# Kernel optimization log

Hardware: AMD Instinct MI355X
Metric: run time of the kernel (lower is better)

## Reference

```python
import jax, jax.numpy as jnp
import numpy as np

WEIGHT = 0.01

def setup_inputs() -> dict:
    key = jax.random.key(0)
    k1, k2 = jax.random.split(key)
    shape = jax.random.normal(k1, (16, 4096, 3), dtype=jnp.float32)
    template = jax.random.normal(k2, (16, 4096, 3), dtype=jnp.float32)
    return {"shape": shape, "template": template}

def _chamfer(pred, target):
    # Euclidean cdist via the |x|^2 + |y|^2 - 2<x,y> expansion to avoid a (B,M,N,3) tensor.
    p2 = jnp.sum(pred * pred, axis=-1)          # (B, M)
    t2 = jnp.sum(target * target, axis=-1)      # (B, N)
    cross = jnp.einsum('bmd,bnd->bmn', pred, target)  # (B, M, N)
    d2 = p2[:, :, None] + t2[None if p2.ndim == 1 else slice(None), None, :] - 2.0 * cross
    dist = jnp.sqrt(jnp.maximum(d2, 0.0))       # (B, M, N) euclidean, matches torch.cdist
    min_p2t = jnp.min(dist, axis=2)             # (B, M)
    min_t2p = jnp.min(dist, axis=1)             # (B, N)
    chamfer = jnp.sum(min_p2t, axis=1) + jnp.sum(min_t2p, axis=1)  # (B,)
    return jnp.mean(chamfer)                    # reduction='mean'

def reference(shape, template):
    return WEIGHT * _chamfer(shape, template)
```

## Files before the change

kernel.cpp:

```cpp
#include <hip/hip_runtime.h>

#define NPTS 4096
#define NBATCH 16
#define THREADS 256
#define QPB 256
#define TCH 1024
#define NCH (NPTS / TCH)

typedef __attribute__((ext_vector_type(8))) short short8;
typedef __attribute__((ext_vector_type(16))) float float16v;

static __device__ __forceinline__ unsigned short f2bf(float f) {
  unsigned int u = __builtin_bit_cast(unsigned int, f);
  u = (u + 0x7FFFu + ((u >> 16) & 1u)) >> 16;
  return (unsigned short)u;
}
static __device__ __forceinline__ float bf2f(unsigned short h) {
  unsigned int u = ((unsigned int)h) << 16;
  return __builtin_bit_cast(float, u);
}
static __device__ __forceinline__ int toff(int j, int h) {
  return (j * 16 + h * 8) ^ (((j >> 2) & 7) << 3);
}

__global__ __launch_bounds__(THREADS)
__attribute__((amdgpu_waves_per_eu(2, 2)))
void chamfer_mfma(const float* __restrict__ shape,
                  const float* __restrict__ tmpl,
                  float* __restrict__ out) {
  __shared__ unsigned short tgt[TCH * 16];
  __shared__ unsigned short qry[QPB * 16];
  __shared__ float p2s[QPB];
  __shared__ float redbuf[4];

  const int qc = blockIdx.x;
  const int b = blockIdx.y;
  const int dir = blockIdx.z;
  const float* Pb = (dir == 0 ? shape : tmpl) + (size_t)b * NPTS * 3;
  const float* Tb = (dir == 0 ? tmpl : shape) + (size_t)b * NPTS * 3;

  const int tid = threadIdx.x;
  const int lane = tid & 63;
  const int wave = tid >> 6;
  const int n = lane & 31;
  const int kg = lane >> 5;

  {
    const int qg = qc * QPB + tid;
    const float px = Pb[3 * qg + 0], py = Pb[3 * qg + 1], pz = Pb[3 * qg + 2];
    const float ux = -2.0f * px, uy = -2.0f * py, uz = -2.0f * pz;
    const unsigned short hx = f2bf(ux), hy = f2bf(uy), hz = f2bf(uz);
    const unsigned short lx = f2bf(ux - bf2f(hx)), ly = f2bf(uy - bf2f(hy)),
                         lz = f2bf(uz - bf2f(hz));
    const unsigned short ONE = 0x3F80;
    short8 v0, v1;
    v0[0] = hx; v0[1] = hx; v0[2] = lx; v0[3] = hy;
    v0[4] = hy; v0[5] = ly; v0[6] = hz; v0[7] = hz;
    v1[0] = lz; v1[1] = ONE; v1[2] = ONE; v1[3] = 0;
    v1[4] = 0;  v1[5] = 0;  v1[6] = 0;  v1[7] = 0;
    *(short8*)&qry[tid * 16] = v0;
    *(short8*)&qry[tid * 16 + 8] = v1;
    p2s[tid] = fmaf(px, px, fmaf(py, py, pz * pz));
  }
  __syncthreads();

  const short8 af0 = *(const short8*)&qry[(wave * 64 + n) * 16 + kg * 8];
  const short8 af1 = *(const short8*)&qry[(wave * 64 + 32 + n) * 16 + kg * 8];

  const float INF = 3.402823466e38f;
  float acc0[16], acc1[16];
  #pragma unroll
  for (int r = 0; r < 16; ++r) { acc0[r] = INF; acc1[r] = INF; }

  const float4* T4 = (const float4*)Tb;
  for (int ch = 0; ch < NCH; ++ch) {
    __syncthreads();
    {
      const int g = ch * (TCH / 4) + tid;
      const float4 a = T4[g * 3 + 0];
      const float4 c = T4[g * 3 + 1];
      const float4 d = T4[g * 3 + 2];
      const float X[4] = {a.x, a.w, c.z, d.y};
      const float Y[4] = {a.y, c.x, c.w, d.z};
      const float Z[4] = {a.z, c.y, d.x, d.w};
      #pragma unroll
      for (int p = 0; p < 4; ++p) {
        const float x = X[p], y = Y[p], z = Z[p];
        const float t2 = fmaf(x, x, fmaf(y, y, z * z));
        const unsigned short hx = f2bf(x), hy = f2bf(y), hz = f2bf(z);
        const unsigned short lx = f2bf(x - bf2f(hx)), ly = f2bf(y - bf2f(hy)),
                             lz = f2bf(z - bf2f(hz));
        const unsigned short h2 = f2bf(t2), l2 = f2bf(t2 - bf2f(h2));
        short8 v0, v1;
        v0[0] = hx; v0[1] = lx; v0[2] = hx; v0[3] = hy;
        v0[4] = ly; v0[5] = hy; v0[6] = hz; v0[7] = lz;
        v1[0] = hz; v1[1] = h2; v1[2] = l2; v1[3] = 0;
        v1[4] = 0;  v1[5] = 0;  v1[6] = 0;  v1[7] = 0;
        const int j = tid * 4 + p;
        *(short8*)&tgt[toff(j, 0)] = v0;
        *(short8*)&tgt[toff(j, 1)] = v1;
      }
    }
    __syncthreads();

    for (int tp = 0; tp < TCH / 64; ++tp) {
      const short8 b0 = *(const short8*)&tgt[toff(tp * 64 + n, kg)];
      const short8 b1 = *(const short8*)&tgt[toff(tp * 64 + 32 + n, kg)];
      const float16v z = {};
      float16v d00 = __builtin_amdgcn_mfma_f32_32x32x16_bf16(af0, b0, z, 0, 0, 0);
      float16v d10 = __builtin_amdgcn_mfma_f32_32x32x16_bf16(af1, b0, z, 0, 0, 0);
      float16v d01 = __builtin_amdgcn_mfma_f32_32x32x16_bf16(af0, b1, z, 0, 0, 0);
      float16v d11 = __builtin_amdgcn_mfma_f32_32x32x16_bf16(af1, b1, z, 0, 0, 0);
      #pragma unroll
      for (int r = 0; r < 16; ++r)
        acc0[r] = fminf(fminf(d00[r], d01[r]), acc0[r]);
      #pragma unroll
      for (int r = 0; r < 16; ++r)
        acc1[r] = fminf(fminf(d10[r], d11[r]), acc1[r]);
    }
  }

  #pragma unroll
  for (int m = 1; m <= 16; m <<= 1) {
    #pragma unroll
    for (int r = 0; r < 16; ++r) {
      acc0[r] = fminf(acc0[r], __shfl_xor(acc0[r], m, 64));
      acc1[r] = fminf(acc1[r], __shfl_xor(acc1[r], m, 64));
    }
  }

  float s = 0.0f;
  if (n == 0) {
    const int qb = wave * 64;
    #pragma unroll
    for (int r = 0; r < 16; ++r) {
      const int row = (r & 3) + 8 * (r >> 2) + 4 * kg;
      s += sqrtf(fmaxf(acc0[r] + p2s[qb + row], 0.0f));
      s += sqrtf(fmaxf(acc1[r] + p2s[qb + 32 + row], 0.0f));
    }
  }
  s += __shfl_xor(s, 32, 64);
  if (lane == 0) redbuf[wave] = s;
  __syncthreads();
  if (tid == 0) {
    atomicAdd(out, (redbuf[0] + redbuf[1] + redbuf[2] + redbuf[3]) * (0.01f / 16.0f));
  }
}

extern "C" void kernel_launch(void* const* d_in, const int* in_sizes, int n_in,
                              void* d_out, int out_size, void* d_ws, size_t ws_size,
                              hipStream_t stream) {
  const float* shape = (const float*)d_in[0];
  const float* tmpl = (const float*)d_in[1];
  float* out = (float*)d_out;

  hipMemsetAsync(out, 0, sizeof(float) * out_size, stream);

  dim3 grid(NPTS / QPB, NBATCH, 2);
  chamfer_mfma<<<grid, dim3(THREADS), 0, stream>>>(shape, tmpl, out);
}
```

Before: 81.88 us.

## Split target set across blocks with workspace combine kernel and fold query norm into MFMA

Splits each query tile's target scan into two halves handled by separate blocks, which doubles the grid. Per-query partial minima go to a workspace, and a second kernel takes the min, applies sqrt, and reduces with a ticket-based last-block sum. This replaces the memset and atomic accumulation. The query norm is folded into the MFMA operands so no p2 add is needed afterwards, and the occupancy hint is raised to 4 waves per EU. A scalar fallback kernel handles the case where the workspace is too small. The change aims to fill the machine better but adds a second launch and workspace traffic.

```diff
diff --git a/kernel.cpp b/kernel.cpp
--- a/kernel.cpp
+++ b/kernel.cpp
@@ -4,8 +4,11 @@
 #define NBATCH 16
 #define THREADS 256
 #define QPB 256
-#define TCH 1024
-#define NCH (NPTS / TCH)
+#define TH 2
+#define TGH (NPTS / TH)
+#define TCH 512
+#define NCH (TGH / TCH)
+#define NBLK_B 512
 
 typedef __attribute__((ext_vector_type(8))) short short8;
 typedef __attribute__((ext_vector_type(16))) float float16v;
@@ -22,18 +25,22 @@
 static __device__ __forceinline__ int toff(int j, int h) {
   return (j * 16 + h * 8) ^ (((j >> 2) & 7) << 3);
 }
+#define WSIDX(b, dir, th, q) (((((b)*2 + (dir)) * 2 + (th)) << 12) + (q))
 
 __global__ __launch_bounds__(THREADS)
-__attribute__((amdgpu_waves_per_eu(2, 2)))
+__attribute__((amdgpu_waves_per_eu(4, 4)))
 void chamfer_mfma(const float* __restrict__ shape,
                   const float* __restrict__ tmpl,
-                  float* __restrict__ out) {
+                  float* __restrict__ ws,
+                  unsigned int* __restrict__ ticket) {
   __shared__ unsigned short tgt[TCH * 16];
   __shared__ unsigned short qry[QPB * 16];
-  __shared__ float p2s[QPB];
-  __shared__ float redbuf[4];
-
-  const int qc = blockIdx.x;
+
+  if (blockIdx.x == 0 && blockIdx.y == 0 && blockIdx.z == 0 && threadIdx.x == 0)
+    *ticket = 0u;
+
+  const int qc = blockIdx.x >> 1;
+  const int th = blockIdx.x & 1;
   const int b = blockIdx.y;
   const int dir = blockIdx.z;
   const float* Pb = (dir == 0 ? shape : tmpl) + (size_t)b * NPTS * 3;
@@ -49,18 +56,19 @@
     const int qg = qc * QPB + tid;
     const float px = Pb[3 * qg + 0], py = Pb[3 * qg + 1], pz = Pb[3 * qg + 2];
     const float ux = -2.0f * px, uy = -2.0f * py, uz = -2.0f * pz;
+    const float p2 = fmaf(px, px, fmaf(py, py, pz * pz));
     const unsigned short hx = f2bf(ux), hy = f2bf(uy), hz = f2bf(uz);
     const unsigned short lx = f2bf(ux - bf2f(hx)), ly = f2bf(uy - bf2f(hy)),
                          lz = f2bf(uz - bf2f(hz));
+    const unsigned short h2 = f2bf(p2), l2 = f2bf(p2 - bf2f(h2));
     const unsigned short ONE = 0x3F80;
     short8 v0, v1;
     v0[0] = hx; v0[1] = hx; v0[2] = lx; v0[3] = hy;
     v0[4] = hy; v0[5] = ly; v0[6] = hz; v0[7] = hz;
-    v1[0] = lz; v1[1] = ONE; v1[2] = ONE; v1[3] = 0;
-    v1[4] = 0;  v1[5] = 0;  v1[6] = 0;  v1[7] = 0;
+    v1[0] = lz; v1[1] = ONE; v1[2] = ONE; v1[3] = h2;
+    v1[4] = l2; v1[5] = 0;  v1[6] = 0;  v1[7] = 0;
     *(short8*)&qry[tid * 16] = v0;
     *(short8*)&qry[tid * 16 + 8] = v1;
-    p2s[tid] = fmaf(px, px, fmaf(py, py, pz * pz));
   }
   __syncthreads();
 
@@ -71,12 +79,13 @@
   float acc0[16], acc1[16];
   #pragma unroll
   for (int r = 0; r < 16; ++r) { acc0[r] = INF; acc1[r] = INF; }
+  const float16v z = {};
 
   const float4* T4 = (const float4*)Tb;
   for (int ch = 0; ch < NCH; ++ch) {
     __syncthreads();
-    {
-      const int g = ch * (TCH / 4) + tid;
+    if (tid < TCH / 4) {
+      const int g = th * (TGH / 4) + ch * (TCH / 4) + tid;
       const float4 a = T4[g * 3 + 0];
       const float4 c = T4[g * 3 + 1];
       const float4 d = T4[g * 3 + 2];
@@ -85,17 +94,18 @@
       const float Z[4] = {a.z, c.y, d.x, d.w};
       #pragma unroll
       for (int p = 0; p < 4; ++p) {
-        const float x = X[p], y = Y[p], z = Z[p];
-        const float t2 = fmaf(x, x, fmaf(y, y, z * z));
-        const unsigned short hx = f2bf(x), hy = f2bf(y), hz = f2bf(z);
+        const float x = X[p], y = Y[p], zc = Z[p];
+        const float t2 = fmaf(x, x, fmaf(y, y, zc * zc));
+        const unsigned short hx = f2bf(x), hy = f2bf(y), hz = f2bf(zc);
         const unsigned short lx = f2bf(x - bf2f(hx)), ly = f2bf(y - bf2f(hy)),
-                             lz = f2bf(z - bf2f(hz));
+                             lz = f2bf(zc - bf2f(hz));
         const unsigned short h2 = f2bf(t2), l2 = f2bf(t2 - bf2f(h2));
+        const unsigned short ONE = 0x3F80;
         short8 v0, v1;
         v0[0] = hx; v0[1] = lx; v0[2] = hx; v0[3] = hy;
         v0[4] = ly; v0[5] = hy; v0[6] = hz; v0[7] = lz;
-        v1[0] = hz; v1[1] = h2; v1[2] = l2; v1[3] = 0;
-        v1[4] = 0;  v1[5] = 0;  v1[6] = 0;  v1[7] = 0;
+        v1[0] = hz; v1[1] = h2; v1[2] = l2; v1[3] = ONE;
+        v1[4] = ONE; v1[5] = 0; v1[6] = 0; v1[7] = 0;
         const int j = tid * 4 + p;
         *(short8*)&tgt[toff(j, 0)] = v0;
         *(short8*)&tgt[toff(j, 1)] = v1;
@@ -103,20 +113,24 @@
     }
     __syncthreads();
 
+    #pragma unroll 2
     for (int tp = 0; tp < TCH / 64; ++tp) {
       const short8 b0 = *(const short8*)&tgt[toff(tp * 64 + n, kg)];
       const short8 b1 = *(const short8*)&tgt[toff(tp * 64 + 32 + n, kg)];
-      const float16v z = {};
-      float16v d00 = __builtin_amdgcn_mfma_f32_32x32x16_bf16(af0, b0, z, 0, 0, 0);
-      float16v d10 = __builtin_amdgcn_mfma_f32_32x32x16_bf16(af1, b0, z, 0, 0, 0);
-      float16v d01 = __builtin_amdgcn_mfma_f32_32x32x16_bf16(af0, b1, z, 0, 0, 0);
-      float16v d11 = __builtin_amdgcn_mfma_f32_32x32x16_bf16(af1, b1, z, 0, 0, 0);
-      #pragma unroll
-      for (int r = 0; r < 16; ++r)
-        acc0[r] = fminf(fminf(d00[r], d01[r]), acc0[r]);
-      #pragma unroll
-      for (int r = 0; r < 16; ++r)
-        acc1[r] = fminf(fminf(d10[r], d11[r]), acc1[r]);
+      {
+        float16v d0 = __builtin_amdgcn_mfma_f32_32x32x16_bf16(af0, b0, z, 0, 0, 0);
+        float16v d1 = __builtin_amdgcn_mfma_f32_32x32x16_bf16(af0, b1, z, 0, 0, 0);
+        #pragma unroll
+        for (int r = 0; r < 16; ++r)
+          acc0[r] = fminf(fminf(d0[r], d1[r]), acc0[r]);
+      }
+      {
+        float16v d0 = __builtin_amdgcn_mfma_f32_32x32x16_bf16(af1, b0, z, 0, 0, 0);
+        float16v d1 = __builtin_amdgcn_mfma_f32_32x32x16_bf16(af1, b1, z, 0, 0, 0);
+        #pragma unroll
+        for (int r = 0; r < 16; ++r)
+          acc1[r] = fminf(fminf(d0[r], d1[r]), acc1[r]);
+      }
     }
   }
 
@@ -129,22 +143,102 @@
     }
   }
 
-  float s = 0.0f;
   if (n == 0) {
-    const int qb = wave * 64;
+    const int qbase = qc * QPB + wave * 64;
+    const int wsb = WSIDX(b, dir, th, 0);
     #pragma unroll
     for (int r = 0; r < 16; ++r) {
       const int row = (r & 3) + 8 * (r >> 2) + 4 * kg;
-      s += sqrtf(fmaxf(acc0[r] + p2s[qb + row], 0.0f));
-      s += sqrtf(fmaxf(acc1[r] + p2s[qb + 32 + row], 0.0f));
-    }
-  }
-  s += __shfl_xor(s, 32, 64);
-  if (lane == 0) redbuf[wave] = s;
-  __syncthreads();
-  if (tid == 0) {
-    atomicAdd(out, (redbuf[0] + redbuf[1] + redbuf[2] + redbuf[3]) * (0.01f / 16.0f));
-  }
+      ws[wsb + qbase + row] = acc0[r];
+      ws[wsb + qbase + 32 + row] = acc1[r];
+    }
+  }
+}
+
+__global__ __launch_bounds__(THREADS) void chamfer_combine(
+    const float* __restrict__ ws, float* __restrict__ partials,
+    unsigned int* __restrict__ ticket, float* __restrict__ out) {
+  __shared__ float red[4];
+  __shared__ bool amLast;
+  const int g = blockIdx.x * THREADS + threadIdx.x;
+  const int b = g >> 13;
+  const int dir = (g >> 12) & 1;
+  const int q = g & 4095;
+
+  const float m = fminf(ws[WSIDX(b, dir, 0, q)], ws[WSIDX(b, dir, 1, q)]);
+  float s = sqrtf(fmaxf(m, 0.0f));
+
+  #pragma unroll
+  for (int off = 32; off > 0; off >>= 1) s += __shfl_down(s, off, 64);
+  const int lane = threadIdx.x & 63;
+  const int wid = threadIdx.x >> 6;
+  if (lane == 0) red[wid] = s;
+  __syncthreads();
+  if (threadIdx.x == 0) {
+    partials[blockIdx.x] = red[0] + red[1] + red[2] + red[3];
+    __threadfence();
+    unsigned int t = atomicAdd(ticket, 1u);
+    amLast = (t == (unsigned int)(gridDim.x - 1));
+  }
+  __syncthreads();
+  if (amLast) {
+    __threadfence();
+    float v = partials[threadIdx.x] + partials[threadIdx.x + THREADS];
+    #pragma unroll
+    for (int off = 32; off > 0; off >>= 1) v += __shfl_down(v, off, 64);
+    if (lane == 0) red[wid] = v;
+    __syncthreads();
+    if (threadIdx.x == 0)
+      out[0] = (red[0] + red[1] + red[2] + red[3]) * (0.01f / 16.0f);
+  }
+}
+
+__global__ __launch_bounds__(THREADS) void chamfer_fallback(
+    const float* __restrict__ shape, const float* __restrict__ tmpl,
+    float* __restrict__ out) {
+  __shared__ float4 tile[NPTS];
+  const int b = blockIdx.y;
+  const int dir = blockIdx.z;
+  const float* Pb = (dir == 0 ? shape : tmpl) + (size_t)b * NPTS * 3;
+  const float* Tb = (dir == 0 ? tmpl : shape) + (size_t)b * NPTS * 3;
+  const float4* T4 = (const float4*)Tb;
+  for (int base = threadIdx.x * 4; base < NPTS; base += THREADS * 4) {
+    const int k = base >> 2;
+    float4 a = T4[3 * k + 0], c = T4[3 * k + 1], d = T4[3 * k + 2];
+    tile[base + 0] = make_float4(a.x, a.y, a.z, 0.5f * fmaf(a.x, a.x, fmaf(a.y, a.y, a.z * a.z)));
+    tile[base + 1] = make_float4(a.w, c.x, c.y, 0.5f * fmaf(a.w, a.w, fmaf(c.x, c.x, c.y * c.y)));
+    tile[base + 2] = make_float4(c.z, c.w, d.x, 0.5f * fmaf(c.z, c.z, fmaf(c.w, c.w, d.x * d.x)));
+    tile[base + 3] = make_float4(d.y, d.z, d.w, 0.5f * fmaf(d.y, d.y, fmaf(d.z, d.z, d.w * d.w)));
+  }
+  __syncthreads();
+  const int m0 = blockIdx.x * (THREADS * 2) + threadIdx.x;
+  const int m1 = m0 + THREADS;
+  const float qx0 = Pb[3 * m0], qy0 = Pb[3 * m0 + 1], qz0 = Pb[3 * m0 + 2];
+  const float qx1 = Pb[3 * m1], qy1 = Pb[3 * m1 + 1], qz1 = Pb[3 * m1 + 2];
+  const float nx0 = -qx0, ny0 = -qy0, nz0 = -qz0;
+  const float nx1 = -qx1, ny1 = -qy1, nz1 = -qz1;
+  const float p20 = fmaf(qx0, qx0, fmaf(qy0, qy0, qz0 * qz0));
+  const float p21 = fmaf(qx1, qx1, fmaf(qy1, qy1, qz1 * qz1));
+  const float INF = 3.402823466e38f;
+  float a00 = INF, a01 = INF, a10 = INF, a11 = INF;
+  #pragma unroll 2
+  for (int n = 0; n < NPTS; n += 2) {
+    float4 t0 = tile[n], t1 = tile[n + 1];
+    a00 = fminf(a00, fmaf(nx0, t0.x, fmaf(ny0, t0.y, fmaf(nz0, t0.z, t0.w))));
+    a10 = fminf(a10, fmaf(nx1, t0.x, fmaf(ny1, t0.y, fmaf(nz1, t0.z, t0.w))));
+    a01 = fminf(a01, fmaf(nx0, t1.x, fmaf(ny0, t1.y, fmaf(nz0, t1.z, t1.w))));
+    a11 = fminf(a11, fmaf(nx1, t1.x, fmaf(ny1, t1.y, fmaf(nz1, t1.z, t1.w))));
+  }
+  float s = sqrtf(fmaxf(fmaf(2.0f, fminf(a00, a01), p20), 0.0f)) +
+            sqrtf(fmaxf(fmaf(2.0f, fminf(a10, a11), p21), 0.0f));
+  #pragma unroll
+  for (int off = 32; off > 0; off >>= 1) s += __shfl_down(s, off, 64);
+  __syncthreads();
+  float* red = (float*)tile;
+  if ((threadIdx.x & 63) == 0) red[threadIdx.x >> 6] = s;
+  __syncthreads();
+  if (threadIdx.x == 0)
+    atomicAdd(out, (red[0] + red[1] + red[2] + red[3]) * (0.01f / 16.0f));
 }
 
 extern "C" void kernel_launch(void* const* d_in, const int* in_sizes, int n_in,
@@ -154,8 +248,19 @@
   const float* tmpl = (const float*)d_in[1];
   float* out = (float*)d_out;
 
-  hipMemsetAsync(out, 0, sizeof(float) * out_size, stream);
-
-  dim3 grid(NPTS / QPB, NBATCH, 2);
-  chamfer_mfma<<<grid, dim3(THREADS), 0, stream>>>(shape, tmpl, out);
-}
+  const size_t ws_mins = (size_t)NBATCH * 2 * TH * NPTS * sizeof(float);
+  const size_t ws_needed = ws_mins + NBLK_B * sizeof(float) + sizeof(unsigned int);
+  if (ws_size >= ws_needed) {
+    float* ws_part = (float*)d_ws;
+    float* partials = (float*)((char*)d_ws + ws_mins);
+    unsigned int* ticket = (unsigned int*)(partials + NBLK_B);
+    dim3 gridA(16 * TH, NBATCH, 2);
+    chamfer_mfma<<<gridA, dim3(THREADS), 0, stream>>>(shape, tmpl, ws_part, ticket);
+    chamfer_combine<<<dim3(NBLK_B), dim3(THREADS), 0, stream>>>(
+        ws_part, partials, ticket, out);
+  } else {
+    hipMemsetAsync(out, 0, sizeof(float) * out_size, stream);
+    dim3 grid(NPTS / (THREADS * 2), NBATCH, 2);
+    chamfer_fallback<<<grid, dim3(THREADS), 0, stream>>>(shape, tmpl, out);
+  }
+}
```

After: 91.30 us. 11.5% more time.

## Halve query tile per block and fold query norm into MFMA K dimension

Applied to the files above, without the earlier changes.

Cuts queries per block from 256 to 128, so each wave handles one 32-row MFMA tile instead of two. This doubles the grid and raises the occupancy target to 4 waves per EU. The query squared norm is now split into hi/lo bf16 terms and placed in spare K slots of the dot-product vector, paired with ONE entries on the target side, so the MFMA output already holds the full squared distance. That removes the p2s shared array and the epilogue add. In exchange, each block stages the full target set into shared memory for half as many queries, which doubles the total target conversion work and LDS traffic.

```diff
diff --git a/kernel.cpp b/kernel.cpp
--- a/kernel.cpp
+++ b/kernel.cpp
@@ -3,7 +3,7 @@
 #define NPTS 4096
 #define NBATCH 16
 #define THREADS 256
-#define QPB 256
+#define QPB 128
 #define TCH 1024
 #define NCH (NPTS / TCH)
 
@@ -24,13 +24,12 @@
 }
 
 __global__ __launch_bounds__(THREADS)
-__attribute__((amdgpu_waves_per_eu(2, 2)))
+__attribute__((amdgpu_waves_per_eu(4, 4)))
 void chamfer_mfma(const float* __restrict__ shape,
                   const float* __restrict__ tmpl,
                   float* __restrict__ out) {
   __shared__ unsigned short tgt[TCH * 16];
   __shared__ unsigned short qry[QPB * 16];
-  __shared__ float p2s[QPB];
   __shared__ float redbuf[4];
 
   const int qc = blockIdx.x;
@@ -45,32 +44,33 @@
   const int n = lane & 31;
   const int kg = lane >> 5;
 
-  {
+  if (tid < QPB) {
     const int qg = qc * QPB + tid;
     const float px = Pb[3 * qg + 0], py = Pb[3 * qg + 1], pz = Pb[3 * qg + 2];
     const float ux = -2.0f * px, uy = -2.0f * py, uz = -2.0f * pz;
+    const float p2 = fmaf(px, px, fmaf(py, py, pz * pz));
     const unsigned short hx = f2bf(ux), hy = f2bf(uy), hz = f2bf(uz);
     const unsigned short lx = f2bf(ux - bf2f(hx)), ly = f2bf(uy - bf2f(hy)),
                          lz = f2bf(uz - bf2f(hz));
+    const unsigned short h2 = f2bf(p2), l2 = f2bf(p2 - bf2f(h2));
     const unsigned short ONE = 0x3F80;
     short8 v0, v1;
     v0[0] = hx; v0[1] = hx; v0[2] = lx; v0[3] = hy;
     v0[4] = hy; v0[5] = ly; v0[6] = hz; v0[7] = hz;
-    v1[0] = lz; v1[1] = ONE; v1[2] = ONE; v1[3] = 0;
-    v1[4] = 0;  v1[5] = 0;  v1[6] = 0;  v1[7] = 0;
+    v1[0] = lz; v1[1] = ONE; v1[2] = ONE; v1[3] = h2;
+    v1[4] = l2; v1[5] = 0;  v1[6] = 0;  v1[7] = 0;
     *(short8*)&qry[tid * 16] = v0;
     *(short8*)&qry[tid * 16 + 8] = v1;
-    p2s[tid] = fmaf(px, px, fmaf(py, py, pz * pz));
   }
   __syncthreads();
 
-  const short8 af0 = *(const short8*)&qry[(wave * 64 + n) * 16 + kg * 8];
-  const short8 af1 = *(const short8*)&qry[(wave * 64 + 32 + n) * 16 + kg * 8];
+  const short8 af = *(const short8*)&qry[(wave * 32 + n) * 16 + kg * 8];
 
   const float INF = 3.402823466e38f;
-  float acc0[16], acc1[16];
+  float acc[16];
   #pragma unroll
-  for (int r = 0; r < 16; ++r) { acc0[r] = INF; acc1[r] = INF; }
+  for (int r = 0; r < 16; ++r) acc[r] = INF;
+  const float16v z = {};
 
   const float4* T4 = (const float4*)Tb;
   for (int ch = 0; ch < NCH; ++ch) {
@@ -85,17 +85,18 @@
       const float Z[4] = {a.z, c.y, d.x, d.w};
       #pragma unroll
       for (int p = 0; p < 4; ++p) {
-        const float x = X[p], y = Y[p], z = Z[p];
-        const float t2 = fmaf(x, x, fmaf(y, y, z * z));
-        const unsigned short hx = f2bf(x), hy = f2bf(y), hz = f2bf(z);
+        const float x = X[p], y = Y[p], zc = Z[p];
+        const float t2 = fmaf(x, x, fmaf(y, y, zc * zc));
+        const unsigned short hx = f2bf(x), hy = f2bf(y), hz = f2bf(zc);
         const unsigned short lx = f2bf(x - bf2f(hx)), ly = f2bf(y - bf2f(hy)),
-                             lz = f2bf(z - bf2f(hz));
+                             lz = f2bf(zc - bf2f(hz));
         const unsigned short h2 = f2bf(t2), l2 = f2bf(t2 - bf2f(h2));
+        const unsigned short ONE = 0x3F80;
         short8 v0, v1;
         v0[0] = hx; v0[1] = lx; v0[2] = hx; v0[3] = hy;
         v0[4] = ly; v0[5] = hy; v0[6] = hz; v0[7] = lz;
-        v1[0] = hz; v1[1] = h2; v1[2] = l2; v1[3] = 0;
-        v1[4] = 0;  v1[5] = 0;  v1[6] = 0;  v1[7] = 0;
+        v1[0] = hz; v1[1] = h2; v1[2] = l2; v1[3] = ONE;
+        v1[4] = ONE; v1[5] = 0; v1[6] = 0; v1[7] = 0;
         const int j = tid * 4 + p;
         *(short8*)&tgt[toff(j, 0)] = v0;
         *(short8*)&tgt[toff(j, 1)] = v1;
@@ -106,38 +107,26 @@
     for (int tp = 0; tp < TCH / 64; ++tp) {
       const short8 b0 = *(const short8*)&tgt[toff(tp * 64 + n, kg)];
       const short8 b1 = *(const short8*)&tgt[toff(tp * 64 + 32 + n, kg)];
-      const float16v z = {};
-      float16v d00 = __builtin_amdgcn_mfma_f32_32x32x16_bf16(af0, b0, z, 0, 0, 0);
-      float16v d10 = __builtin_amdgcn_mfma_f32_32x32x16_bf16(af1, b0, z, 0, 0, 0);
-      float16v d01 = __builtin_amdgcn_mfma_f32_32x32x16_bf16(af0, b1, z, 0, 0, 0);
-      float16v d11 = __builtin_amdgcn_mfma_f32_32x32x16_bf16(af1, b1, z, 0, 0, 0);
+      float16v d0 = __builtin_amdgcn_mfma_f32_32x32x16_bf16(af, b0, z, 0, 0, 0);
+      float16v d1 = __builtin_amdgcn_mfma_f32_32x32x16_bf16(af, b1, z, 0, 0, 0);
       #pragma unroll
       for (int r = 0; r < 16; ++r)
-        acc0[r] = fminf(fminf(d00[r], d01[r]), acc0[r]);
-      #pragma unroll
-      for (int r = 0; r < 16; ++r)
-        acc1[r] = fminf(fminf(d10[r], d11[r]), acc1[r]);
+        acc[r] = fminf(fminf(d0[r], d1[r]), acc[r]);
     }
   }
 
   #pragma unroll
   for (int m = 1; m <= 16; m <<= 1) {
     #pragma unroll
-    for (int r = 0; r < 16; ++r) {
-      acc0[r] = fminf(acc0[r], __shfl_xor(acc0[r], m, 64));
-      acc1[r] = fminf(acc1[r], __shfl_xor(acc1[r], m, 64));
-    }
+    for (int r = 0; r < 16; ++r)
+      acc[r] = fminf(acc[r], __shfl_xor(acc[r], m, 64));
   }
 
   float s = 0.0f;
   if (n == 0) {
-    const int qb = wave * 64;
     #pragma unroll
-    for (int r = 0; r < 16; ++r) {
-      const int row = (r & 3) + 8 * (r >> 2) + 4 * kg;
-      s += sqrtf(fmaxf(acc0[r] + p2s[qb + row], 0.0f));
-      s += sqrtf(fmaxf(acc1[r] + p2s[qb + 32 + row], 0.0f));
-    }
+    for (int r = 0; r < 16; ++r)
+      s += sqrtf(fmaxf(acc[r], 0.0f));
   }
   s += __shfl_xor(s, 32, 64);
   if (lane == 0) redbuf[wave] = s;
```

Result: no change. 81.33 us (-0.7%).

## Precompute bf16 split records in a prep kernel and stream targets from global

Applied to the files above, without the earlier changes.

Adds a prep kernel that converts every point once into both query-side and target-side bf16 hi/lo MFMA records in workspace, folding the query norm into the MFMA through extra K lanes. The main kernel then reads target fragments directly from global/L2 instead of staging and converting them in LDS per block, which removes the barriers, the LDS traffic and the repeated conversion work. This costs an extra launch and 4 MB of workspace traffic, and loses LDS reuse, so it relies on L2 bandwidth. A scalar fp32 fallback kernel runs when the workspace is too small.

```diff
diff --git a/kernel.cpp b/kernel.cpp
--- a/kernel.cpp
+++ b/kernel.cpp
@@ -4,11 +4,10 @@
 #define NBATCH 16
 #define THREADS 256
 #define QPB 256
-#define TCH 1024
-#define NCH (NPTS / TCH)
 
 typedef __attribute__((ext_vector_type(8))) short short8;
 typedef __attribute__((ext_vector_type(16))) float float16v;
+typedef unsigned short ushort_t;
 
 static __device__ __forceinline__ unsigned short f2bf(float f) {
   unsigned int u = __builtin_bit_cast(unsigned int, f);
@@ -19,25 +18,63 @@
   unsigned int u = ((unsigned int)h) << 16;
   return __builtin_bit_cast(float, u);
 }
-static __device__ __forceinline__ int toff(int j, int h) {
-  return (j * 16 + h * 8) ^ (((j >> 2) & 7) << 3);
+
+
+__global__ __launch_bounds__(THREADS) void chamfer_prep(
+    const float* __restrict__ shape, const float* __restrict__ tmpl,
+    ushort_t* __restrict__ Arec, ushort_t* __restrict__ Brec) {
+  const int i = blockIdx.x * THREADS + threadIdx.x;
+  const int b = blockIdx.y;
+  const int src = blockIdx.z;
+  const float* P = (src == 0 ? shape : tmpl) + ((size_t)b * NPTS + i) * 3;
+  const float x = P[0], y = P[1], zc = P[2];
+  const unsigned short ONE = 0x3F80;
+
+  const size_t idx = ((size_t)(src * NBATCH + b) * NPTS + i) * 16;
+
+  {
+    const float ux = -2.0f * x, uy = -2.0f * y, uz = -2.0f * zc;
+    const float p2 = fmaf(x, x, fmaf(y, y, zc * zc));
+    const unsigned short hx = f2bf(ux), hy = f2bf(uy), hz = f2bf(uz);
+    const unsigned short lx = f2bf(ux - bf2f(hx)), ly = f2bf(uy - bf2f(hy)),
+                         lz = f2bf(uz - bf2f(hz));
+    const unsigned short h2 = f2bf(p2), l2 = f2bf(p2 - bf2f(h2));
+    short8 v0, v1;
+    v0[0] = hx; v0[1] = hx; v0[2] = lx; v0[3] = hy;
+    v0[4] = hy; v0[5] = ly; v0[6] = hz; v0[7] = hz;
+    v1[0] = lz; v1[1] = ONE; v1[2] = ONE; v1[3] = h2;
+    v1[4] = l2; v1[5] = 0;  v1[6] = 0;  v1[7] = 0;
+    *(short8*)&Arec[idx] = v0;
+    *(short8*)&Arec[idx + 8] = v1;
+  }
+  {
+    const float t2 = fmaf(x, x, fmaf(y, y, zc * zc));
+    const unsigned short hx = f2bf(x), hy = f2bf(y), hz = f2bf(zc);
+    const unsigned short lx = f2bf(x - bf2f(hx)), ly = f2bf(y - bf2f(hy)),
+                         lz = f2bf(zc - bf2f(hz));
+    const unsigned short h2 = f2bf(t2), l2 = f2bf(t2 - bf2f(h2));
+    short8 v0, v1;
+    v0[0] = hx; v0[1] = lx; v0[2] = hx; v0[3] = hy;
+    v0[4] = ly; v0[5] = hy; v0[6] = hz; v0[7] = lz;
+    v1[0] = hz; v1[1] = h2; v1[2] = l2; v1[3] = ONE;
+    v1[4] = ONE; v1[5] = 0; v1[6] = 0; v1[7] = 0;
+    *(short8*)&Brec[idx] = v0;
+    *(short8*)&Brec[idx + 8] = v1;
+  }
 }
 
 __global__ __launch_bounds__(THREADS)
 __attribute__((amdgpu_waves_per_eu(2, 2)))
-void chamfer_mfma(const float* __restrict__ shape,
-                  const float* __restrict__ tmpl,
+void chamfer_main(const ushort_t* __restrict__ Arec,
+                  const ushort_t* __restrict__ Brec,
                   float* __restrict__ out) {
-  __shared__ unsigned short tgt[TCH * 16];
-  __shared__ unsigned short qry[QPB * 16];
-  __shared__ float p2s[QPB];
   __shared__ float redbuf[4];
 
   const int qc = blockIdx.x;
   const int b = blockIdx.y;
   const int dir = blockIdx.z;
-  const float* Pb = (dir == 0 ? shape : tmpl) + (size_t)b * NPTS * 3;
-  const float* Tb = (dir == 0 ? tmpl : shape) + (size_t)b * NPTS * 3;
+  const ushort_t* Ab = Arec + ((size_t)(dir * NBATCH + b) * NPTS) * 16;
+  const ushort_t* Bb = Brec + ((size_t)((1 - dir) * NBATCH + b) * NPTS) * 16;
 
   const int tid = threadIdx.x;
   const int lane = tid & 63;
@@ -45,79 +82,32 @@
   const int n = lane & 31;
   const int kg = lane >> 5;
 
-  {
-    const int qg = qc * QPB + tid;
-    const float px = Pb[3 * qg + 0], py = Pb[3 * qg + 1], pz = Pb[3 * qg + 2];
-    const float ux = -2.0f * px, uy = -2.0f * py, uz = -2.0f * pz;
-    const unsigned short hx = f2bf(ux), hy = f2bf(uy), hz = f2bf(uz);
-    const unsigned short lx = f2bf(ux - bf2f(hx)), ly = f2bf(uy - bf2f(hy)),
-                         lz = f2bf(uz - bf2f(hz));
-    const unsigned short ONE = 0x3F80;
-    short8 v0, v1;
-    v0[0] = hx; v0[1] = hx; v0[2] = lx; v0[3] = hy;
-    v0[4] = hy; v0[5] = ly; v0[6] = hz; v0[7] = hz;
-    v1[0] = lz; v1[1] = ONE; v1[2] = ONE; v1[3] = 0;
-    v1[4] = 0;  v1[5] = 0;  v1[6] = 0;  v1[7] = 0;
-    *(short8*)&qry[tid * 16] = v0;
-    *(short8*)&qry[tid * 16 + 8] = v1;
-    p2s[tid] = fmaf(px, px, fmaf(py, py, pz * pz));
-  }
-  __syncthreads();
-
-  const short8 af0 = *(const short8*)&qry[(wave * 64 + n) * 16 + kg * 8];
-  const short8 af1 = *(const short8*)&qry[(wave * 64 + 32 + n) * 16 + kg * 8];
+  const int qb = qc * QPB + wave * 64;
+  const short8 af0 = *(const short8*)(Ab + (size_t)(qb + n) * 16 + kg * 8);
+  const short8 af1 = *(const short8*)(Ab + (size_t)(qb + 32 + n) * 16 + kg * 8);
 
   const float INF = 3.402823466e38f;
   float acc0[16], acc1[16];
   #pragma unroll
   for (int r = 0; r < 16; ++r) { acc0[r] = INF; acc1[r] = INF; }
-
-  const float4* T4 = (const float4*)Tb;
-  for (int ch = 0; ch < NCH; ++ch) {
-    __syncthreads();
-    {
-      const int g = ch * (TCH / 4) + tid;
-      const float4 a = T4[g * 3 + 0];
-      const float4 c = T4[g * 3 + 1];
-      const float4 d = T4[g * 3 + 2];
-      const float X[4] = {a.x, a.w, c.z, d.y};
-      const float Y[4] = {a.y, c.x, c.w, d.z};
-      const float Z[4] = {a.z, c.y, d.x, d.w};
-      #pragma unroll
-      for (int p = 0; p < 4; ++p) {
-        const float x = X[p], y = Y[p], z = Z[p];
-        const float t2 = fmaf(x, x, fmaf(y, y, z * z));
-        const unsigned short hx = f2bf(x), hy = f2bf(y), hz = f2bf(z);
-        const unsigned short lx = f2bf(x - bf2f(hx)), ly = f2bf(y - bf2f(hy)),
-                             lz = f2bf(z - bf2f(hz));
-        const unsigned short h2 = f2bf(t2), l2 = f2bf(t2 - bf2f(h2));
-        short8 v0, v1;
-        v0[0] = hx; v0[1] = lx; v0[2] = hx; v0[3] = hy;
-        v0[4] = ly; v0[5] = hy; v0[6] = hz; v0[7] = lz;
-        v1[0] = hz; v1[1] = h2; v1[2] = l2; v1[3] = 0;
-        v1[4] = 0;  v1[5] = 0;  v1[6] = 0;  v1[7] = 0;
-        const int j = tid * 4 + p;
-        *(short8*)&tgt[toff(j, 0)] = v0;
-        *(short8*)&tgt[toff(j, 1)] = v1;
-      }
-    }
-    __syncthreads();
-
-    for (int tp = 0; tp < TCH / 64; ++tp) {
-      const short8 b0 = *(const short8*)&tgt[toff(tp * 64 + n, kg)];
-      const short8 b1 = *(const short8*)&tgt[toff(tp * 64 + 32 + n, kg)];
-      const float16v z = {};
-      float16v d00 = __builtin_amdgcn_mfma_f32_32x32x16_bf16(af0, b0, z, 0, 0, 0);
-      float16v d10 = __builtin_amdgcn_mfma_f32_32x32x16_bf16(af1, b0, z, 0, 0, 0);
-      float16v d01 = __builtin_amdgcn_mfma_f32_32x32x16_bf16(af0, b1, z, 0, 0, 0);
-      float16v d11 = __builtin_amdgcn_mfma_f32_32x32x16_bf16(af1, b1, z, 0, 0, 0);
-      #pragma unroll
-      for (int r = 0; r < 16; ++r)
-        acc0[r] = fminf(fminf(d00[r], d01[r]), acc0[r]);
-      #pragma unroll
-      for (int r = 0; r < 16; ++r)
-        acc1[r] = fminf(fminf(d10[r], d11[r]), acc1[r]);
-    }
+  const float16v z = {};
+
+  const ushort_t* bp = Bb + n * 16 + kg * 8;
+
+  #pragma unroll 4
+  for (int tp = 0; tp < NPTS / 64; ++tp) {
+    const short8 b0 = *(const short8*)(bp + tp * 1024);
+    const short8 b1 = *(const short8*)(bp + tp * 1024 + 512);
+    const float16v d00 = __builtin_amdgcn_mfma_f32_32x32x16_bf16(af0, b0, z, 0, 0, 0);
+    const float16v d01 = __builtin_amdgcn_mfma_f32_32x32x16_bf16(af0, b1, z, 0, 0, 0);
+    const float16v d10 = __builtin_amdgcn_mfma_f32_32x32x16_bf16(af1, b0, z, 0, 0, 0);
+    const float16v d11 = __builtin_amdgcn_mfma_f32_32x32x16_bf16(af1, b1, z, 0, 0, 0);
+    #pragma unroll
+    for (int r = 0; r < 16; ++r)
+      acc0[r] = fminf(fminf(d00[r], d01[r]), acc0[r]);
+    #pragma unroll
+    for (int r = 0; r < 16; ++r)
+      acc1[r] = fminf(fminf(d10[r], d11[r]), acc1[r]);
   }
 
   #pragma unroll
@@ -131,12 +121,10 @@
 
   float s = 0.0f;
   if (n == 0) {
-    const int qb = wave * 64;
     #pragma unroll
     for (int r = 0; r < 16; ++r) {
-      const int row = (r & 3) + 8 * (r >> 2) + 4 * kg;
-      s += sqrtf(fmaxf(acc0[r] + p2s[qb + row], 0.0f));
-      s += sqrtf(fmaxf(acc1[r] + p2s[qb + 32 + row], 0.0f));
+      s += sqrtf(fmaxf(acc0[r], 0.0f));
+      s += sqrtf(fmaxf(acc1[r], 0.0f));
     }
   }
   s += __shfl_xor(s, 32, 64);
@@ -145,6 +133,54 @@
   if (tid == 0) {
     atomicAdd(out, (redbuf[0] + redbuf[1] + redbuf[2] + redbuf[3]) * (0.01f / 16.0f));
   }
+}
+
+__global__ __launch_bounds__(THREADS) void chamfer_fallback(
+    const float* __restrict__ shape, const float* __restrict__ tmpl,
+    float* __restrict__ out) {
+  __shared__ float4 tile[NPTS];
+  const int b = blockIdx.y;
+  const int dir = blockIdx.z;
+  const float* Pb = (dir == 0 ? shape : tmpl) + (size_t)b * NPTS * 3;
+  const float* Tb = (dir == 0 ? tmpl : shape) + (size_t)b * NPTS * 3;
+  const float4* T4 = (const float4*)Tb;
+  for (int base = threadIdx.x * 4; base < NPTS; base += THREADS * 4) {
+    const int k = base >> 2;
+    float4 a = T4[3 * k + 0], c = T4[3 * k + 1], d = T4[3 * k + 2];
+    tile[base + 0] = make_float4(a.x, a.y, a.z, 0.5f * fmaf(a.x, a.x, fmaf(a.y, a.y, a.z * a.z)));
+    tile[base + 1] = make_float4(a.w, c.x, c.y, 0.5f * fmaf(a.w, a.w, fmaf(c.x, c.x, c.y * c.y)));
+    tile[base + 2] = make_float4(c.z, c.w, d.x, 0.5f * fmaf(c.z, c.z, fmaf(c.w, c.w, d.x * d.x)));
+    tile[base + 3] = make_float4(d.y, d.z, d.w, 0.5f * fmaf(d.y, d.y, fmaf(d.z, d.z, d.w * d.w)));
+  }
+  __syncthreads();
+  const int m0 = blockIdx.x * (THREADS * 2) + threadIdx.x;
+  const int m1 = m0 + THREADS;
+  const float qx0 = Pb[3 * m0], qy0 = Pb[3 * m0 + 1], qz0 = Pb[3 * m0 + 2];
+  const float qx1 = Pb[3 * m1], qy1 = Pb[3 * m1 + 1], qz1 = Pb[3 * m1 + 2];
+  const float nx0 = -qx0, ny0 = -qy0, nz0 = -qz0;
+  const float nx1 = -qx1, ny1 = -qy1, nz1 = -qz1;
+  const float p20 = fmaf(qx0, qx0, fmaf(qy0, qy0, qz0 * qz0));
+  const float p21 = fmaf(qx1, qx1, fmaf(qy1, qy1, qz1 * qz1));
+  const float INF = 3.402823466e38f;
+  float a00 = INF, a01 = INF, a10 = INF, a11 = INF;
+  #pragma unroll 2
+  for (int n = 0; n < NPTS; n += 2) {
+    float4 t0 = tile[n], t1 = tile[n + 1];
+    a00 = fminf(a00, fmaf(nx0, t0.x, fmaf(ny0, t0.y, fmaf(nz0, t0.z, t0.w))));
+    a10 = fminf(a10, fmaf(nx1, t0.x, fmaf(ny1, t0.y, fmaf(nz1, t0.z, t0.w))));
+    a01 = fminf(a01, fmaf(nx0, t1.x, fmaf(ny0, t1.y, fmaf(nz0, t1.z, t1.w))));
+    a11 = fminf(a11, fmaf(nx1, t1.x, fmaf(ny1, t1.y, fmaf(nz1, t1.z, t1.w))));
+  }
+  float s = sqrtf(fmaxf(fmaf(2.0f, fminf(a00, a01), p20), 0.0f)) +
+            sqrtf(fmaxf(fmaf(2.0f, fminf(a10, a11), p21), 0.0f));
+  #pragma unroll
+  for (int off = 32; off > 0; off >>= 1) s += __shfl_down(s, off, 64);
+  __syncthreads();
+  float* red = (float*)tile;
+  if ((threadIdx.x & 63) == 0) red[threadIdx.x >> 6] = s;
+  __syncthreads();
+  if (threadIdx.x == 0)
+    atomicAdd(out, (red[0] + red[1] + red[2] + red[3]) * (0.01f / 16.0f));
 }
 
 extern "C" void kernel_launch(void* const* d_in, const int* in_sizes, int n_in,
@@ -156,6 +192,16 @@
 
   hipMemsetAsync(out, 0, sizeof(float) * out_size, stream);
 
-  dim3 grid(NPTS / QPB, NBATCH, 2);
-  chamfer_mfma<<<grid, dim3(THREADS), 0, stream>>>(shape, tmpl, out);
-}
+  const size_t rec_bytes = (size_t)2 * NBATCH * NPTS * 32;
+  if (ws_size >= 2 * rec_bytes) {
+    ushort_t* Arec = (ushort_t*)d_ws;
+    ushort_t* Brec = (ushort_t*)((char*)d_ws + rec_bytes);
+    chamfer_prep<<<dim3(NPTS / THREADS, NBATCH, 2), dim3(THREADS), 0, stream>>>(
+        shape, tmpl, Arec, Brec);
+    chamfer_main<<<dim3(NPTS / QPB, NBATCH, 2), dim3(THREADS), 0, stream>>>(
+        Arec, Brec, out);
+  } else {
+    dim3 grid(NPTS / (THREADS * 2), NBATCH, 2);
+    chamfer_fallback<<<grid, dim3(THREADS), 0, stream>>>(shape, tmpl, out);
+  }
+}
```

Result: slower. 87.92 us (+7.4%).
